# Kernel tuning notes

Measured on AMD Instinct MI355X. Metric: run time of the kernel, lower is better.

Reference implementation:

```python
import jax, jax.numpy as jnp
import numpy as np

B, S, H, D = 4, 2048, 12, 64
HIDDEN = H * D  # 768
WINDOW = 64     # config.local_attention // 2
ROPE_THETA = 10000.0  # local_rope_theta for sliding layers


def rotate_half(x):
    d = x.shape[-1] // 2
    return jnp.concatenate([-x[..., d:], x[..., :d]], axis=-1)


def setup_inputs() -> dict:
    key = jax.random.key(0)
    k1, k2, k3 = jax.random.split(key, 3)
    hidden_states = jax.random.normal(k1, (B, S, HIDDEN), dtype=jnp.float32)
    # RoPE tables (HF style): inv_freq over half dims, duplicated
    inv_freq = 1.0 / (ROPE_THETA ** (jnp.arange(0, D, 2, dtype=jnp.float32) / D))  # [D/2]
    pos = jnp.arange(S, dtype=jnp.float32)
    freqs = pos[:, None] * inv_freq[None, :]          # [S, D/2]
    emb = jnp.concatenate([freqs, freqs], axis=-1)    # [S, D]
    cos = jnp.broadcast_to(jnp.cos(emb)[None], (B, S, D))
    sin = jnp.broadcast_to(jnp.sin(emb)[None], (B, S, D))
    # sliding-window additive mask [B,1,S,S]
    idx = jnp.arange(S)
    allowed = jnp.abs(idx[:, None] - idx[None, :]) <= WINDOW
    neg = jnp.finfo(jnp.float32).min
    attention_mask = jnp.broadcast_to(
        jnp.where(allowed, 0.0, neg)[None, None], (B, 1, S, S)
    ).astype(jnp.float32)
    std = 0.02
    Wqkv_w = jax.random.normal(k2, (3 * HIDDEN, HIDDEN), dtype=jnp.float32) * std
    Wo_w = jax.random.normal(k3, (HIDDEN, HIDDEN), dtype=jnp.float32) * std
    return {"hidden_states": hidden_states, "cos": cos, "sin": sin,
            "attention_mask": attention_mask, "Wqkv_w": Wqkv_w, "Wo_w": Wo_w}


def reference(hidden_states, cos, sin, attention_mask, Wqkv_w, Wo_w):
    b, s, _ = hidden_states.shape
    scaling = D ** -0.5
    qkv = hidden_states @ Wqkv_w.T                       # [B,S,3*HIDDEN]
    qkv = qkv.reshape(b, s, 3, H, D)
    q = jnp.transpose(qkv[:, :, 0], (0, 2, 1, 3))        # [B,H,S,D]
    k = jnp.transpose(qkv[:, :, 1], (0, 2, 1, 3))
    v = jnp.transpose(qkv[:, :, 2], (0, 2, 1, 3))
    # RoPE with float32 intermediates (inputs already fp32 here)
    c = cos[:, None].astype(jnp.float32)                 # [B,1,S,D]
    sn = sin[:, None].astype(jnp.float32)
    qf, kf = q.astype(jnp.float32), k.astype(jnp.float32)
    q = (qf * c + rotate_half(qf) * sn).astype(q.dtype)
    k = (kf * c + rotate_half(kf) * sn).astype(k.dtype)
    # SDPA with explicit additive mask
    scores = jnp.einsum('bhqd,bhkd->bhqk', q, k) * scaling + attention_mask
    attn = jax.nn.softmax(scores, axis=-1)
    out = jnp.einsum('bhqk,bhkd->bhqd', attn, v)         # [B,H,S,D]
    out = jnp.transpose(out, (0, 2, 1, 3)).reshape(b, s, HIDDEN)
    return out @ Wo_w.T
```

## Files before the change

kernel.cpp:

```cpp
#include <hip/hip_runtime.h>
#include <math.h>


typedef __attribute__((ext_vector_type(8))) short short8;
typedef __attribute__((ext_vector_type(4))) float floatx4;

constexpr int kB = 4;
constexpr int kS = 2048;
constexpr int kH = 12;
constexpr int kD = 64;
constexpr int kHidden = 768;
constexpr int kQKV = 3 * kHidden;

__device__ __forceinline__ unsigned short f2bf(float f) {
  union { float f; unsigned int u; } x; x.f = f;
  unsigned int r = (x.u + 0x7fffu + ((x.u >> 16) & 1u)) >> 16;
  return (unsigned short)r;
}

__global__ __launch_bounds__(256) void cvt_all(
    const float* __restrict__ h, const float* __restrict__ wqkv,
    const float* __restrict__ wo, unsigned short* __restrict__ hb,
    unsigned short* __restrict__ wqb, unsigned short* __restrict__ wob) {
  constexpr int n1 = kB * kS * kHidden / 4;
  constexpr int n2 = kQKV * kHidden / 4;
  constexpr int n3 = kHidden * kHidden / 4;
  int i = blockIdx.x * 256 + threadIdx.x;
  const float* src;
  unsigned short* dst;
  if (i < n1) {
    src = h; dst = hb;
  } else if (i < n1 + n2) {
    i -= n1; src = wqkv; dst = wqb;
  } else {
    i -= n1 + n2; if (i >= n3) return; src = wo; dst = wob;
  }
  const float4 v = ((const float4*)src)[i];
  ushort4 o;
  o.x = f2bf(v.x); o.y = f2bf(v.y); o.z = f2bf(v.z); o.w = f2bf(v.w);
  ((ushort4*)dst)[i] = o;
}

__device__ __forceinline__ void gload_lds16(const unsigned short* g, unsigned short* l) {
  __builtin_amdgcn_global_load_lds(
      (const __attribute__((address_space(1))) unsigned int*)g,
      (__attribute__((address_space(3))) unsigned int*)l, 16, 0, 0);
}

__global__ __launch_bounds__(256) void gemm_qkv(
    const unsigned short* __restrict__ A,
    const unsigned short* __restrict__ B,
    const float* __restrict__ cosp, const float* __restrict__ sinp,
    unsigned short* __restrict__ Qr, unsigned short* __restrict__ Kr,
    unsigned short* __restrict__ Vt) {
  constexpr int K = kHidden;
  __shared__ unsigned short SH[128 * 136];
  unsigned short* As = SH;
  unsigned short* Bs = SH + 128 * 64;

  const int tid = threadIdx.x;
  const int lane = tid & 63;
  const int wave = tid >> 6;
  const int m0 = blockIdx.x * 128;
  const int n0 = blockIdx.y * 128;

  int ldsS[4];
  const unsigned short* gA[4];
  const unsigned short* gB[4];
#pragma unroll
  for (int t = 0; t < 4; t++) {
    const int ci = (wave * 4 + t) * 64 + lane;
    const int row = ci >> 3;
    const int c = (ci & 7) ^ (row & 7);
    ldsS[t] = ci * 8;
    gA[t] = A + (size_t)(m0 + row) * K + c * 8;
    gB[t] = B + (size_t)(n0 + row) * K + c * 8;
  }

  const int wm = wave >> 1, wn = wave & 1;
  const int mr = wm * 64 + (lane & 15);
  const int nr = wn * 64 + (lane & 15);
  const int kq = lane >> 4;

  floatx4 acc[4][4];
#pragma unroll
  for (int i = 0; i < 4; i++)
#pragma unroll
    for (int j = 0; j < 4; j++) acc[i][j] = (floatx4)(0.f);

  for (int k0 = 0; k0 < K; k0 += 64) {
    if (k0) __syncthreads();
#pragma unroll
    for (int t = 0; t < 4; t++) {
      gload_lds16(gA[t] + k0, &As[ldsS[t]]);
      gload_lds16(gB[t] + k0, &Bs[ldsS[t]]);
    }
    __syncthreads();
#pragma unroll
    for (int s = 0; s < 2; s++) {
      short8 af[4], bf[4];
#pragma unroll
      for (int i = 0; i < 4; i++) {
        af[i] = *(const short8*)&As[(mr + i * 16) * 64 + (((s * 4 + kq) ^ (mr & 7)) * 8)];
        bf[i] = *(const short8*)&Bs[(nr + i * 16) * 64 + (((s * 4 + kq) ^ (nr & 7)) * 8)];
      }
#pragma unroll
      for (int i = 0; i < 4; i++)
#pragma unroll
        for (int j = 0; j < 4; j++)
          acc[i][j] = __builtin_amdgcn_mfma_f32_16x16x32_bf16(af[i], bf[j],
                                                              acc[i][j], 0, 0, 0);
    }
  }

  __syncthreads();
  unsigned short (*Obuf)[136] = (unsigned short (*)[136])SH;

  const int region = n0 / kHidden;
  const int b = m0 >> 11, s0 = m0 & 2047;
  const int h0 = (n0 % kHidden) >> 6;
  const int rowL0 = wm * 64 + kq * 4;

  if (region == 2) {
#pragma unroll
    for (int i = 0; i < 4; i++)
#pragma unroll
      for (int r = 0; r < 4; r++) {
        const int rowL = rowL0 + i * 16 + r;
#pragma unroll
        for (int j = 0; j < 4; j++)
          Obuf[wn * 64 + j * 16 + (lane & 15)][rowL] = f2bf(acc[i][j][r]);
      }
    __syncthreads();
#pragma unroll
    for (int it = 0; it < 8; it++) {
      const int t = tid + it * 256;
      const int s8 = t & 15, rowc = t >> 4;
      const int hl = rowc >> 6, d = rowc & 63;
      *(short8*)(Vt + ((size_t)(b * kH + h0 + hl) * kD + d) * kS + s0 + s8 * 8) =
          *(const short8*)&Obuf[rowc][s8 * 8];
    }
  } else {
    unsigned short* dst = (region == 0) ? Qr : Kr;
    const float qscale = (region == 0) ? 0.125f : 1.f;
#pragma unroll
    for (int i = 0; i < 4; i++)
#pragma unroll
      for (int r = 0; r < 4; r++) {
        const int rowL = rowL0 + i * 16 + r;
        const int s = s0 + rowL;
        const float* cs = cosp + ((size_t)(b * kS + s)) * kD;
        const float* sns = sinp + ((size_t)(b * kS + s)) * kD;
#pragma unroll
        for (int jp = 0; jp < 2; jp++) {
          const int colL = wn * 64 + jp * 16 + (lane & 15);
          const int d = colL & 63;
          const float c = cs[d], sn = sns[d];
          const float xlo = acc[i][jp][r], xhi = acc[i][jp + 2][r];
          Obuf[rowL][colL]      = f2bf((xlo * c - xhi * sn) * qscale);
          Obuf[rowL][colL + 32] = f2bf((xhi * c + xlo * sn) * qscale);
        }
      }
    __syncthreads();
#pragma unroll
    for (int it = 0; it < 8; it++) {
      const int t = tid + it * 256;
      const int d8 = t & 7, sl = (t >> 3) & 127, hl = t >> 10;
      *(short8*)(dst + ((size_t)(b * kH + h0 + hl) * kS + s0 + sl) * kD + d8 * 8) =
          *(const short8*)&Obuf[sl][hl * 64 + d8 * 8];
    }
  }
}

__global__ __launch_bounds__(256) void gemm_bf16_nt(
    const unsigned short* __restrict__ A, const unsigned short* __restrict__ B,
    float* __restrict__ C, int M, int N, int K) {
  __shared__ unsigned short As[128 * 64];
  __shared__ unsigned short Bs[128 * 64];

  const int tid = threadIdx.x;
  const int lane = tid & 63;
  const int wave = tid >> 6;
  const int m0 = blockIdx.x * 128;
  const int n0 = blockIdx.y * 128;

  int ldsS[4];
  const unsigned short* gA[4];
  const unsigned short* gB[4];
#pragma unroll
  for (int t = 0; t < 4; t++) {
    const int ci = (wave * 4 + t) * 64 + lane;
    const int row = ci >> 3;
    const int c = (ci & 7) ^ (row & 7);
    ldsS[t] = ci * 8;
    gA[t] = A + (size_t)(m0 + row) * K + c * 8;
    gB[t] = B + (size_t)(n0 + row) * K + c * 8;
  }

  const int wm = wave >> 1, wn = wave & 1;
  const int mr = wm * 64 + (lane & 15);
  const int nr = wn * 64 + (lane & 15);
  const int kq = lane >> 4;

  floatx4 acc[4][4];
#pragma unroll
  for (int i = 0; i < 4; i++)
#pragma unroll
    for (int j = 0; j < 4; j++) acc[i][j] = (floatx4)(0.f);

  for (int k0 = 0; k0 < K; k0 += 64) {
    if (k0) __syncthreads();
#pragma unroll
    for (int t = 0; t < 4; t++) {
      gload_lds16(gA[t] + k0, &As[ldsS[t]]);
      gload_lds16(gB[t] + k0, &Bs[ldsS[t]]);
    }
    __syncthreads();
#pragma unroll
    for (int s = 0; s < 2; s++) {
      short8 af[4], bf[4];
#pragma unroll
      for (int i = 0; i < 4; i++) {
        af[i] = *(const short8*)&As[(mr + i * 16) * 64 + (((s * 4 + kq) ^ (mr & 7)) * 8)];
        bf[i] = *(const short8*)&Bs[(nr + i * 16) * 64 + (((s * 4 + kq) ^ (nr & 7)) * 8)];
      }
#pragma unroll
      for (int i = 0; i < 4; i++)
#pragma unroll
        for (int j = 0; j < 4; j++)
          acc[i][j] = __builtin_amdgcn_mfma_f32_16x16x32_bf16(af[i], bf[j],
                                                              acc[i][j], 0, 0, 0);
    }
  }

  const int crow = m0 + wm * 64 + kq * 4;
  const int ccol = n0 + wn * 64 + (lane & 15);
#pragma unroll
  for (int i = 0; i < 4; i++)
#pragma unroll
    for (int r = 0; r < 4; r++) {
      float* cp = C + (size_t)(crow + i * 16 + r) * N + ccol;
#pragma unroll
      for (int j = 0; j < 4; j++) cp[j * 16] = acc[i][j][r];
    }
}

constexpr int AQT = 32;

__global__ __launch_bounds__(256) void attn_v3(
    const unsigned short* __restrict__ Qr, const unsigned short* __restrict__ Kr,
    const unsigned short* __restrict__ Vt, unsigned short* __restrict__ out) {
  __shared__ unsigned short Pfrag[2][5][64][8];
  __shared__ float Ssum[2][AQT];

  const int tid = threadIdx.x;
  const int lane = tid & 63;
  const int wave = tid >> 6;
  const int quad = lane >> 4;
  const int l15 = lane & 15;
  const int qbase = blockIdx.x * AQT;
  const int h = blockIdx.y, b = blockIdx.z;
  const int bh = b * kH + h;
  const int kbase = qbase - 64;
  const int tq = wave >> 1;
  const int kh = wave & 1;

  short8 vf[2][5];
  {
    const unsigned short* vbase = Vt + (size_t)bh * kD * kS;
#pragma unroll
    for (int nt = 0; nt < 2; nt++) {
      const unsigned short* vrow = vbase + (size_t)(kh * 32 + nt * 16 + l15) * kS;
#pragma unroll
      for (int kk = 0; kk < 5; kk++) {
        int s0 = kbase + kk * 32 + quad * 8;
        s0 = min(max(s0, 0), kS - 8);
        vf[nt][kk] = *(const short8*)(vrow + s0);
      }
    }
  }

  const unsigned short* qsrc =
      Qr + ((size_t)bh * kS + qbase + tq * 16 + l15) * kD + quad * 8;
  const short8 a0 = *(const short8*)qsrc;
  const short8 a1 = *(const short8*)(qsrc + 32);

  floatx4 acc[5];
  const unsigned short* ksrc = Kr + (size_t)bh * kS * kD;
#pragma unroll
  for (int g = 0; g < 5; g++) {
    int row = kbase + (kh * 5 + g) * 16 + l15;
    row = min(max(row, 0), kS - 1);
    const unsigned short* kp = ksrc + (size_t)row * kD + quad * 8;
    const short8 b0 = *(const short8*)kp;
    const short8 b1 = *(const short8*)(kp + 32);
    floatx4 z = (floatx4)(0.f);
    z = __builtin_amdgcn_mfma_f32_16x16x32_bf16(a0, b0, z, 0, 0, 0);
    z = __builtin_amdgcn_mfma_f32_16x16x32_bf16(a1, b1, z, 0, 0, 0);
    acc[g] = z;
  }

#pragma unroll
  for (int r = 0; r < 4; r++) {
    const int q = tq * 16 + quad * 4 + r;
    float s = 0.f;
#pragma unroll
    for (int g = 0; g < 5; g++) {
      const int key = (kh * 5 + g) * 16 + l15;
      const int kg_ = kbase + key;
      const bool valid = (key >= q) && (key <= q + 128) && (kg_ >= 0) && (kg_ < kS);
      const float e = valid ? __expf(acc[g][r]) : 0.f;
      s += e;
      Pfrag[tq][key >> 5][((key >> 3) & 3) * 16 + quad * 4 + r][key & 7] = f2bf(e);
    }
#pragma unroll
    for (int off = 1; off < 16; off <<= 1) s += __shfl_xor(s, off, 64);
    if (l15 == 0) Ssum[kh][q] = s;
  }
  __syncthreads();

  floatx4 o0 = (floatx4)(0.f), o1 = (floatx4)(0.f);
#pragma unroll
  for (int kk = 0; kk < 5; kk++) {
    const short8 pa = *(const short8*)&Pfrag[tq][kk][lane][0];
    o0 = __builtin_amdgcn_mfma_f32_16x16x32_bf16(pa, vf[0][kk], o0, 0, 0, 0);
    o1 = __builtin_amdgcn_mfma_f32_16x16x32_bf16(pa, vf[1][kk], o1, 0, 0, 0);
  }

#pragma unroll
  for (int r = 0; r < 4; r++) {
    const int q = tq * 16 + quad * 4 + r;
    const float inv = 1.f / (Ssum[0][q] + Ssum[1][q]);
    unsigned short* op =
        out + ((size_t)(b * kS + qbase + q)) * kHidden + h * kD + kh * 32 + l15;
    op[0] = f2bf(o0[r] * inv);
    op[16] = f2bf(o1[r] * inv);
  }
}

extern "C" void kernel_launch(void* const* d_in, const int* in_sizes, int n_in,
                              void* d_out, int out_size, void* d_ws,
                              size_t ws_size, hipStream_t stream) {
  const float* hidden = (const float*)d_in[0];
  const float* cosp = (const float*)d_in[1];
  const float* sinp = (const float*)d_in[2];
  const float* wqkv = (const float*)d_in[4];
  const float* wo = (const float*)d_in[5];
  float* out = (float*)d_out;

  const int M = kB * kS;
  const size_t szH = (size_t)M * kHidden;

  unsigned short* hbf = (unsigned short*)d_ws;
  unsigned short* wqkvbf = hbf + szH;
  unsigned short* wobf = wqkvbf + (size_t)kQKV * kHidden;
  unsigned short* attnbf = wobf + (size_t)kHidden * kHidden;
  unsigned short* Qrb = attnbf + szH;
  unsigned short* Krb = Qrb + szH;
  unsigned short* Vtb = Krb + szH;

  const int ncvt = (M * kHidden + kQKV * kHidden + kHidden * kHidden) / 4;
  cvt_all<<<(ncvt + 255) / 256, 256, 0, stream>>>(hidden, wqkv, wo, hbf,
                                                  wqkvbf, wobf);

  dim3 g1(M / 128, kQKV / 128);
  gemm_qkv<<<g1, 256, 0, stream>>>(hbf, wqkvbf, cosp, sinp, Qrb, Krb, Vtb);

  dim3 ga(kS / AQT, kH, kB);
  attn_v3<<<ga, 256, 0, stream>>>(Qrb, Krb, Vtb, attnbf);

  dim3 g2(M / 128, kHidden / 128);
  gemm_bf16_nt<<<g2, 256, 0, stream>>>(attnbf, wobf, out, M, kHidden, kHidden);
}
```

Measured before the change: 210.9 us.

## Double attention query tile and store Q/K token-major from the QKV GEMM

Result: slower. 215.6 us (+2.2%).

```diff
diff --git a/kernel.cpp b/kernel.cpp
--- a/kernel.cpp
+++ b/kernel.cpp
@@ -118,7 +118,8 @@
 
   const int region = n0 / kHidden;
   const int b = m0 >> 11, s0 = m0 & 2047;
-  const int h0 = (n0 % kHidden) >> 6;
+  const int n0c = n0 % kHidden;
+  const int h0 = n0c >> 6;
   const int rowL0 = wm * 64 + kq * 4;
 
   if (region == 2) {
@@ -165,9 +166,9 @@
 #pragma unroll
     for (int it = 0; it < 8; it++) {
       const int t = tid + it * 256;
-      const int d8 = t & 7, sl = (t >> 3) & 127, hl = t >> 10;
-      *(short8*)(dst + ((size_t)(b * kH + h0 + hl) * kS + s0 + sl) * kD + d8 * 8) =
-          *(const short8*)&Obuf[sl][hl * 64 + d8 * 8];
+      const int c8 = t & 15, rowL = t >> 4;
+      *(short8*)(dst + ((size_t)(b * kS + s0 + rowL)) * kHidden + n0c + c8 * 8) =
+          *(const short8*)&Obuf[rowL][c8 * 8];
     }
   }
 }
@@ -245,12 +246,12 @@
     }
 }
 
-constexpr int AQT = 32;
-
-__global__ __launch_bounds__(256) void attn_v3(
+constexpr int AQT = 64;
+
+__global__ __launch_bounds__(512, 4) void attn_v4(
     const unsigned short* __restrict__ Qr, const unsigned short* __restrict__ Kr,
     const unsigned short* __restrict__ Vt, unsigned short* __restrict__ out) {
-  __shared__ unsigned short Pfrag[2][5][64][8];
+  __shared__ unsigned short Pfrag[4][6][64][8];
   __shared__ float Ssum[2][AQT];
 
   const int tid = threadIdx.x;
@@ -260,19 +261,18 @@
   const int l15 = lane & 15;
   const int qbase = blockIdx.x * AQT;
   const int h = blockIdx.y, b = blockIdx.z;
-  const int bh = b * kH + h;
   const int kbase = qbase - 64;
   const int tq = wave >> 1;
   const int kh = wave & 1;
 
-  short8 vf[2][5];
+  short8 vf[2][6];
   {
-    const unsigned short* vbase = Vt + (size_t)bh * kD * kS;
+    const unsigned short* vbase = Vt + (size_t)(b * kH + h) * kD * kS;
 #pragma unroll
     for (int nt = 0; nt < 2; nt++) {
       const unsigned short* vrow = vbase + (size_t)(kh * 32 + nt * 16 + l15) * kS;
 #pragma unroll
-      for (int kk = 0; kk < 5; kk++) {
+      for (int kk = 0; kk < 6; kk++) {
         int s0 = kbase + kk * 32 + quad * 8;
         s0 = min(max(s0, 0), kS - 8);
         vf[nt][kk] = *(const short8*)(vrow + s0);
@@ -281,17 +281,17 @@
   }
 
   const unsigned short* qsrc =
-      Qr + ((size_t)bh * kS + qbase + tq * 16 + l15) * kD + quad * 8;
+      Qr + ((size_t)(b * kS) + qbase + tq * 16 + l15) * kHidden + h * kD + quad * 8;
   const short8 a0 = *(const short8*)qsrc;
   const short8 a1 = *(const short8*)(qsrc + 32);
 
-  floatx4 acc[5];
-  const unsigned short* ksrc = Kr + (size_t)bh * kS * kD;
-#pragma unroll
-  for (int g = 0; g < 5; g++) {
-    int row = kbase + (kh * 5 + g) * 16 + l15;
+  floatx4 acc[6];
+  const unsigned short* ksrc = Kr + (size_t)(b * kS) * kHidden + h * kD;
+#pragma unroll
+  for (int g = 0; g < 6; g++) {
+    int row = kbase + (kh * 6 + g) * 16 + l15;
     row = min(max(row, 0), kS - 1);
-    const unsigned short* kp = ksrc + (size_t)row * kD + quad * 8;
+    const unsigned short* kp = ksrc + (size_t)row * kHidden + quad * 8;
     const short8 b0 = *(const short8*)kp;
     const short8 b1 = *(const short8*)(kp + 32);
     floatx4 z = (floatx4)(0.f);
@@ -302,26 +302,28 @@
 
 #pragma unroll
   for (int r = 0; r < 4; r++) {
-    const int q = tq * 16 + quad * 4 + r;
+    const int ql = tq * 16 + quad * 4 + r;
     float s = 0.f;
 #pragma unroll
-    for (int g = 0; g < 5; g++) {
-      const int key = (kh * 5 + g) * 16 + l15;
+    for (int g = 0; g < 6; g++) {
+      const int key = (kh * 6 + g) * 16 + l15;
       const int kg_ = kbase + key;
-      const bool valid = (key >= q) && (key <= q + 128) && (kg_ >= 0) && (kg_ < kS);
+      const int qrel = quad * 4 + r + tq * 16;
+      const bool valid =
+          (key >= qrel) && (key <= qrel + 128) && (kg_ >= 0) && (kg_ < kS);
       const float e = valid ? __expf(acc[g][r]) : 0.f;
       s += e;
       Pfrag[tq][key >> 5][((key >> 3) & 3) * 16 + quad * 4 + r][key & 7] = f2bf(e);
     }
 #pragma unroll
     for (int off = 1; off < 16; off <<= 1) s += __shfl_xor(s, off, 64);
-    if (l15 == 0) Ssum[kh][q] = s;
+    if (l15 == 0) Ssum[kh][ql] = s;
   }
   __syncthreads();
 
   floatx4 o0 = (floatx4)(0.f), o1 = (floatx4)(0.f);
 #pragma unroll
-  for (int kk = 0; kk < 5; kk++) {
+  for (int kk = 0; kk < 6; kk++) {
     const short8 pa = *(const short8*)&Pfrag[tq][kk][lane][0];
     o0 = __builtin_amdgcn_mfma_f32_16x16x32_bf16(pa, vf[0][kk], o0, 0, 0, 0);
     o1 = __builtin_amdgcn_mfma_f32_16x16x32_bf16(pa, vf[1][kk], o1, 0, 0, 0);
@@ -329,10 +331,10 @@
 
 #pragma unroll
   for (int r = 0; r < 4; r++) {
-    const int q = tq * 16 + quad * 4 + r;
-    const float inv = 1.f / (Ssum[0][q] + Ssum[1][q]);
+    const int ql = tq * 16 + quad * 4 + r;
+    const float inv = 1.f / (Ssum[0][ql] + Ssum[1][ql]);
     unsigned short* op =
-        out + ((size_t)(b * kS + qbase + q)) * kHidden + h * kD + kh * 32 + l15;
+        out + ((size_t)(b * kS + qbase + ql)) * kHidden + h * kD + kh * 32 + l15;
     op[0] = f2bf(o0[r] * inv);
     op[16] = f2bf(o1[r] * inv);
   }
@@ -367,7 +369,7 @@
   gemm_qkv<<<g1, 256, 0, stream>>>(hbf, wqkvbf, cosp, sinp, Qrb, Krb, Vtb);
 
   dim3 ga(kS / AQT, kH, kB);
-  attn_v3<<<ga, 256, 0, stream>>>(Qrb, Krb, Vtb, attnbf);
+  attn_v4<<<ga, 512, 0, stream>>>(Qrb, Krb, Vtb, attnbf);
 
   dim3 g2(M / 128, kHidden / 128);
   gemm_bf16_nt<<<g2, 256, 0, stream>>>(attnbf, wobf, out, M, kHidden, kHidden);
```
